# Optimization experiments

Measured on AMD Instinct MI355X. Metric: run time of the kernel, lower is better.

The kernel has to match this reference:

```python
import jax, jax.numpy as jnp
import numpy as np

N = 6144      # nodes
DIN = 65      # input_dim (1 time + 64 space coords)
DOUT = 65     # output_dim per head
H = 4         # nheads
EPS = 1e-7
MIN = 1e-15
# curvature c = 1 throughout (MultiHeadGraphAttentionLayer hardcodes curvature=1)

def arcosh(z):
    return jnp.log(z + jnp.sqrt(jnp.maximum(z * z - 1.0, 0.0)))

def hyp_proj(u):
    # project onto hyperboloid: recompute time coord
    y = u[..., 1:]
    t = jnp.sqrt(1.0 + jnp.sum(y * y, -1, keepdims=True))
    return jnp.concatenate([t, y], -1)

def expmap0(u):
    v = u[..., 1:]
    n = jnp.maximum(jnp.linalg.norm(v, axis=-1, keepdims=True), MIN)
    return jnp.concatenate([jnp.cosh(n), jnp.sinh(n) * v / n], -1)

def logmap0(x):
    y = x[..., 1:]
    n = jnp.maximum(jnp.linalg.norm(y, axis=-1, keepdims=True), MIN)
    t = jnp.maximum(x[..., :1], 1.0 + EPS)
    return jnp.concatenate([jnp.zeros_like(t), arcosh(t) * y / n], -1)

def hyp_linear(x, W):
    # HypLinear (use_bias=False, eval mode): mobius_matvec = exp0(log0(x) @ W^T), then proj
    return hyp_proj(expmap0(logmap0(x) @ W.T))

def to_poincare(x):
    return x[..., 1:] / (x[..., :1] + 1.0)

def to_hyperboloid(p):
    s = jnp.sum(p * p, -1, keepdims=True)
    return jnp.concatenate([1.0 + s, 2.0 * p], -1) / jnp.maximum(1.0 - s, MIN)

def mobius_half(v):
    # 0.5 (x) v  (mobius scalar multiplication, c=1)
    n = jnp.maximum(jnp.linalg.norm(v, axis=-1, keepdims=True), MIN)
    return jnp.tanh(0.5 * jnp.arctanh(jnp.minimum(n, 1.0 - EPS))) * v / n

def head(x, adj_t, Wa, Wd, Wo):
    att = hyp_linear(x, Wa)   # [N, DOUT]
    red = hyp_linear(x, Wd)   # [N, DOUT]
    # pairwise hyperboloid sqdist via Minkowski inner product (negate time coord)
    am = att.at[:, 0].multiply(-1.0)
    theta = jnp.maximum(-(am @ att.T), 1.0 + EPS)          # [N, N]
    S = jnp.minimum(arcosh(theta) ** 2, 50.0)
    # coef[i, j] = -adj[j, i] * sqdist for incoming edges (mask = adj^T)
    coef = jnp.where(adj_t > 0.01, -adj_t * S, 0.0)
    # F.normalize along incoming-edge axis (zeros don't change the L2 norm)
    a = coef / jnp.maximum(jnp.linalg.norm(coef, axis=-1, keepdims=True), 1e-12)
    pv = to_poincare(red)                                   # [N, DOUT-1]
    lam = 2.0 / jnp.maximum(1.0 - jnp.sum(pv * pv, -1), MIN)  # conformal factors [N]
    num = (a * lam[None, :]) @ pv                           # [N, DOUT-1]
    den = jnp.sum(jnp.abs(a) * (lam - 1.0)[None, :], -1, keepdims=True)
    m = mobius_half(num / jnp.maximum(den, MIN))            # mobius midpoint
    return hyp_linear(to_hyperboloid(m), Wo)                # [N, DOUT]

def reference(x, adj, W_att, W_data, W_out, W_lin):
    adj_t = adj.T
    hs = jnp.stack([head(x, adj_t, W_att[h], W_data[h], W_out[h]) for h in range(H)], axis=1)  # [N, H, DOUT]
    p = to_poincare(hs).reshape(x.shape[0], -1)             # PoincareBall.concat -> [N, H*(DOUT-1)]
    return hyp_linear(to_hyperboloid(p), W_lin)             # [N, H*DOUT]

def setup_inputs():
    key = jax.random.key(0)
    ks = jax.random.split(key, 8)
    sp = 0.1 * jax.random.normal(ks[0], (N, DIN - 1), jnp.float32)
    x = jnp.concatenate([jnp.sqrt(1.0 + jnp.sum(sp * sp, -1, keepdims=True)), sp], -1)
    adj = (jax.random.uniform(ks[1], (N, N)) < 32.0 / N).astype(jnp.float32)
    adj = jnp.maximum(adj, jnp.eye(N, dtype=jnp.float32))  # every node >=1 incoming edge
    def xavier(k, shape):
        b = (6.0 / (shape[0] + shape[1])) ** 0.5
        return jax.random.uniform(k, shape, jnp.float32, -b, b)
    W_att = jnp.stack([xavier(jax.random.fold_in(ks[2], h), (DOUT, DIN)) for h in range(H)])
    W_data = jnp.stack([xavier(jax.random.fold_in(ks[3], h), (DOUT, DIN)) for h in range(H)])
    W_out = jnp.stack([xavier(jax.random.fold_in(ks[4], h), (DOUT, DOUT)) for h in range(H)])
    W_lin = xavier(ks[5], (H * DOUT, H * (DOUT - 1) + 1))
    return {"x": x, "adj": adj, "W_att": W_att, "W_data": W_data, "W_out": W_out, "W_lin": W_lin}
```

## Files before the change

kernel.cpp:

```cpp
#include <hip/hip_runtime.h>
#include <math.h>

#define N 6144
#define H 4
#define CAP 128
#define MINF 1e-15f
#define ONE_EPS  1.0000001192092896f
#define ONE_MEPS 0.9999998807907104f

__device__ __forceinline__ float wave_reduce_sum(float v) {
    v += __shfl_xor(v, 32, 64);
    v += __shfl_xor(v, 16, 64);
    v += __shfl_xor(v, 8, 64);
    v += __shfl_xor(v, 4, 64);
    v += __shfl_xor(v, 2, 64);
    v += __shfl_xor(v, 1, 64);
    return v;
}

__device__ __forceinline__ float arcosh_f(float z) {
    return logf(z + sqrtf(fmaxf(z * z - 1.0f, 0.0f)));
}

__global__ void k_prep(const float* __restrict__ x, float* __restrict__ lmv,
                       const float* __restrict__ W_att, const float* __restrict__ W_data,
                       const float* __restrict__ W_out, const float* __restrict__ Wl,
                       float* __restrict__ Bp, float* __restrict__ Bo,
                       float* __restrict__ WlT, int* __restrict__ cnt) {
    int b = blockIdx.x;
    if (b < 1536) {
        int i = b * 4 + (threadIdx.x >> 6);
        int lane = threadIdx.x & 63;
        float y = x[i * 65 + 1 + lane];
        float ss = wave_reduce_sum(y * y);
        float n = fmaxf(sqrtf(ss), MINF);
        float t = fmaxf(x[i * 65], ONE_EPS);
        lmv[i * 64 + lane] = arcosh_f(t) * y / n;
    } else if (b < 1728) {
        int tid = (b - 1536) * 256 + threadIdx.x;
        int m = tid >> 12;
        int r = tid & 4095;
        int k = r >> 6, o = r & 63;
        const float* src;
        if (m < 4) src = W_att + m * 65 * 65;
        else if (m < 8) src = W_data + (m - 4) * 65 * 65;
        else src = W_out + (m - 8) * 65 * 65;
        float val = src[(1 + o) * 65 + (1 + k)];
        if (m < 8) Bp[m * 4096 + k * 64 + o] = val;
        else Bo[(m - 8) * 4096 + k * 64 + o] = val;
    } else if (b < 1808) {
        int L = ((b - 1728) * 256 + threadIdx.x) * 4;
        int k = L / 320, o0 = L % 320;
        float v[4];
        #pragma unroll
        for (int q = 0; q < 4; q++) {
            int o = o0 + q;
            v[q] = (o < 259) ? Wl[(size_t)(1 + o) * 257 + 1 + k] : 0.f;
        }
        *(float4*)(WlT + L) = make_float4(v[0], v[1], v[2], v[3]);
    } else {
        cnt[(b - 1808) * 256 + threadIdx.x] = 0;
    }
}

__global__ void __launch_bounds__(256) k_csr_gemm(
        const float* __restrict__ adj, int* __restrict__ cnt, int* __restrict__ idx,
        const float* __restrict__ lmv, const float* __restrict__ Bp,
        float* __restrict__ attv, float2* __restrict__ a0l, float* __restrict__ pv) {
    __shared__ float smem[64 * 65];
    if (blockIdx.x < 768) {
        float (*As)[64] = (float(*)[64])smem;
        float (*Bs)[64] = (float(*)[64])(smem + 1024);
        float (*Cs)[65] = (float(*)[65])smem;
        int my = blockIdx.x / 96;
        int ix = blockIdx.x % 96;
        const float* Bb = Bp + (size_t)my * 4096;
        int i0 = ix * 64;
        int tid = threadIdx.x;
        int tx = tid & 15, ty = tid >> 4;
        float acc[4][4] = {};
        for (int k0 = 0; k0 < 64; k0 += 16) {
            {
                int mm = tid >> 2, kq = tid & 3;
                float4 v = *(const float4*)(lmv + (size_t)(i0 + mm) * 64 + k0 + kq * 4);
                As[kq * 4 + 0][mm] = v.x;
                As[kq * 4 + 1][mm] = v.y;
                As[kq * 4 + 2][mm] = v.z;
                As[kq * 4 + 3][mm] = v.w;
            }
            {
                int kk = tid >> 4, o4 = tid & 15;
                float4 bvv = *(const float4*)(Bb + (k0 + kk) * 64 + o4 * 4);
                *(float4*)&Bs[kk][o4 * 4] = bvv;
            }
            __syncthreads();
            #pragma unroll
            for (int kk = 0; kk < 16; kk++) {
                float4 av = *(const float4*)&As[kk][ty * 4];
                float4 bv = *(const float4*)&Bs[kk][tx * 4];
                float a[4] = {av.x, av.y, av.z, av.w};
                float b[4] = {bv.x, bv.y, bv.z, bv.w};
                #pragma unroll
                for (int r = 0; r < 4; r++)
                    #pragma unroll
                    for (int c = 0; c < 4; c++) acc[r][c] += a[r] * b[c];
            }
            __syncthreads();
        }
        #pragma unroll
        for (int r = 0; r < 4; r++)
            #pragma unroll
            for (int c = 0; c < 4; c++)
                Cs[ty * 4 + r][tx * 4 + c] = acc[r][c];
        __syncthreads();
        int w = tid >> 6, lane = tid & 63;
        bool isAtt = my < 4;
        int h = my & 3;
        #pragma unroll 1
        for (int r = 0; r < 16; r++) {
            int row = w * 16 + r;
            int i = i0 + row;
            float u = Cs[row][lane];
            float nn = fmaxf(sqrtf(wave_reduce_sum(u * u)), MINF);
            if (isAtt) {
                float sha = sinhf(nn);
                attv[((size_t)h * N + i) * 64 + lane] = sha * u / nn;
                if (lane == 0) a0l[h * N + i].x = coshf(nn);
            } else {
                float shd = sinhf(nn), chd = coshf(nn);
                float pvd = (shd * u / nn) / (chd + 1.0f);
                pv[((size_t)h * N + i) * 64 + lane] = pvd;
                float sp = wave_reduce_sum(pvd * pvd);
                if (lane == 0) a0l[h * N + i].y = 2.0f / fmaxf(1.0f - sp, MINF);
            }
        }
    } else {
        const float4* a4 = (const float4*)adj;
        const unsigned STRIDE = 1048576u;
        unsigned e0 = (blockIdx.x - 768) * 256 + threadIdx.x;
        float4 v0 = a4[e0];
        float4 v1 = a4[e0 + STRIDE];
        #pragma unroll 1
        for (int it = 0; it < 9; it++) {
            float4 vn;
            if (it < 7) vn = a4[e0 + (unsigned)(it + 2) * STRIDE];
            unsigned base = (e0 + (unsigned)it * STRIDE) * 4u;
            float vals[4] = {v0.x, v0.y, v0.z, v0.w};
            #pragma unroll
            for (int q = 0; q < 4; q++) {
                if (vals[q] > 0.01f) {
                    unsigned t = base + q;
                    int j = t / N;
                    int i = t % N;
                    int pos = atomicAdd(&cnt[i], 1);
                    if (pos < CAP) idx[i * CAP + pos] = j;
                }
            }
            v0 = v1;
            v1 = vn;
        }
    }
}

__global__ void __launch_bounds__(256) k_attn(
        const int* __restrict__ cnt, const int* __restrict__ idx,
        const float* __restrict__ attv, const float2* __restrict__ a0l,
        const float* __restrict__ pv, float* __restrict__ lm2) {
    __shared__ float wls[4][CAP];
    __shared__ int jls[4][CAP];
    int w = threadIdx.x >> 6, lane = threadIdx.x & 63;
    int i = blockIdx.x * 4 + w;
    int h = blockIdx.y;
    const float* attvh = attv + (size_t)h * N * 64;
    const float* pvh = pv + (size_t)h * N * 64;
    const float2* a0lh = a0l + (size_t)h * N;

    int c = lane & 3;
    float4 aireg[4];
    #pragma unroll
    for (int q = 0; q < 4; q++)
        aireg[q] = *(const float4*)(attvh + (size_t)i * 64 + q * 16 + c * 4);
    float ai0 = a0lh[i].x;
    int nn = min(cnt[i], CAP);

    float accd = 0.f, accss = 0.f;
    for (int base = 0; base < nn; base += 16) {
        int t = base + (lane >> 2);
        bool act = t < nn;
        int j = act ? idx[i * CAP + t] : i;
        float2 al = a0lh[j];
        float d = 0.f;
        #pragma unroll
        for (int q = 0; q < 4; q++) {
            float4 b = *(const float4*)(attvh + (size_t)j * 64 + q * 16 + c * 4);
            float4 a = aireg[q];
            d += a.x * b.x + a.y * b.y + a.z * b.z + a.w * b.w;
        }
        d += __shfl_xor(d, 1, 64);
        d += __shfl_xor(d, 2, 64);
        float theta = fmaxf(ai0 * al.x - d, ONE_EPS);
        float ar = arcosh_f(theta);
        float S = fminf(ar * ar, 50.0f);
        if (!act) S = 0.f;
        if (c == 0) {
            accd += S * (al.y - 1.0f);
            accss += S * S;
            wls[w][t] = S * al.y;
            jls[w][t] = j;
        }
    }
    accd = wave_reduce_sum(accd);
    accss = wave_reduce_sum(accss);
    float nrm = fmaxf(sqrtf(accss), 1e-12f);
    float den = fmaxf(accd / nrm, MINF);
    float scl = 1.0f / (nrm * den);

    float accn = 0.f;
    #pragma unroll 4
    for (int t = 0; t < nn; t++) {
        int j = jls[w][t];
        float wq = wls[w][t];
        accn = fmaf(wq, pvh[(size_t)j * 64 + lane], accn);
    }
    float v = -scl * accn;
    float nv = fmaxf(sqrtf(wave_reduce_sum(v * v)), MINF);
    float nc = fminf(nv, ONE_MEPS);
    float mh = tanhf(0.5f * atanhf(nc));
    float md = mh * v / nv;
    float s = wave_reduce_sum(md * md);
    float Dh = fmaxf(1.0f - s, MINF);
    float hb0 = (1.0f + s) / Dh;
    float hbv = 2.0f * md / Dh;
    float nh = fmaxf(2.0f * sqrtf(s) / Dh, MINF);
    float t2 = fmaxf(hb0, ONE_EPS);
    lm2[((size_t)h * N + i) * 64 + lane] = arcosh_f(t2) * hbv / nh;
}

#define PS 272
#define BS5 336
__global__ void __launch_bounds__(256) k_tail(
        const float* __restrict__ lm2, const float* __restrict__ Bo,
        const float* __restrict__ WlT, float* __restrict__ out) {
    __shared__ float smem[5376 + 16 * PS];
    float* As1 = smem;
    float* Bs1 = smem + 1088;
    float* Bs5 = smem;
    float* P   = smem + 5376;

    int i0 = blockIdx.x * 16;
    int tid = threadIdx.x;
    int ty = tid >> 4;
    int tx = tid & 15;

    for (int h = 0; h < H; h++) {
        {
            float4 v = *(const float4*)(lm2 + ((size_t)h * N + i0 + ty) * 64 + tx * 4);
            *(float4*)(As1 + ty * 68 + tx * 4) = v;
        }
        float acc[4] = {0.f, 0.f, 0.f, 0.f};
        for (int k0 = 0; k0 < 64; k0 += 16) {
            {
                *(float4*)(Bs1 + ty * 64 + tx * 4) =
                    *(const float4*)(Bo + (size_t)h * 4096 + (k0 + ty) * 64 + tx * 4);
            }
            __syncthreads();
            #pragma unroll
            for (int kk = 0; kk < 16; kk++) {
                float a = As1[ty * 68 + k0 + kk];
                float4 bv = *(const float4*)(Bs1 + kk * 64 + tx * 4);
                acc[0] += a * bv.x;
                acc[1] += a * bv.y;
                acc[2] += a * bv.z;
                acc[3] += a * bv.w;
            }
            __syncthreads();
        }
        float ss = acc[0] * acc[0] + acc[1] * acc[1] + acc[2] * acc[2] + acc[3] * acc[3];
        ss += __shfl_xor(ss, 1, 64);
        ss += __shfl_xor(ss, 2, 64);
        ss += __shfl_xor(ss, 4, 64);
        ss += __shfl_xor(ss, 8, 64);
        float nn = fmaxf(sqrtf(ss), MINF);
        float sh = sinhf(nn), ch = coshf(nn);
        float* Pr = P + ty * PS + h * 64 + tx * 4;
        Pr[0] = (sh * acc[0] / nn) / (ch + 1.0f);
        Pr[1] = (sh * acc[1] / nn) / (ch + 1.0f);
        Pr[2] = (sh * acc[2] / nn) / (ch + 1.0f);
        Pr[3] = (sh * acc[3] / nn) / (ch + 1.0f);
    }
    __syncthreads();

    {
        float sp = 0.f;
        float4 pl[4];
        #pragma unroll
        for (int q = 0; q < 4; q++) {
            pl[q] = *(const float4*)(P + ty * PS + q * 64 + tx * 4);
            sp += pl[q].x * pl[q].x + pl[q].y * pl[q].y
                + pl[q].z * pl[q].z + pl[q].w * pl[q].w;
        }
        sp += __shfl_xor(sp, 1, 64);
        sp += __shfl_xor(sp, 2, 64);
        sp += __shfl_xor(sp, 4, 64);
        sp += __shfl_xor(sp, 8, 64);
        float Dh = fmaxf(1.0f - sp, MINF);
        float t2 = fmaxf((1.0f + sp) / Dh, ONE_EPS);
        float nh = fmaxf(2.0f * sqrtf(sp) / Dh, MINF);
        float ar2 = arcosh_f(t2);
        #pragma unroll
        for (int q = 0; q < 4; q++) {
            float4 v = pl[q];
            v.x = ar2 * (2.0f * v.x / Dh) / nh;
            v.y = ar2 * (2.0f * v.y / Dh) / nh;
            v.z = ar2 * (2.0f * v.z / Dh) / nh;
            v.w = ar2 * (2.0f * v.w / Dh) / nh;
            *(float4*)(P + ty * PS + q * 64 + tx * 4) = v;
        }
    }
    __syncthreads();

    float acc2[5][4] = {};
    for (int k0 = 0; k0 < 256; k0 += 16) {
        {
            #pragma unroll
            for (int q = 0; q < 5; q++)
                *(float4*)(Bs5 + ty * BS5 + q * 64 + tx * 4) =
                    *(const float4*)(WlT + (size_t)(k0 + ty) * 320 + q * 64 + tx * 4);
        }
        __syncthreads();
        #pragma unroll
        for (int kq = 0; kq < 4; kq++) {
            float4 pv4 = *(const float4*)(P + ty * PS + k0 + kq * 4);
            float av[4] = {pv4.x, pv4.y, pv4.z, pv4.w};
            #pragma unroll
            for (int j = 0; j < 4; j++) {
                float a = av[j];
                int kk = kq * 4 + j;
                #pragma unroll
                for (int q = 0; q < 5; q++) {
                    float4 bv = *(const float4*)(Bs5 + kk * BS5 + q * 64 + tx * 4);
                    acc2[q][0] += a * bv.x;
                    acc2[q][1] += a * bv.y;
                    acc2[q][2] += a * bv.z;
                    acc2[q][3] += a * bv.w;
                }
            }
        }
        __syncthreads();
    }

    float ss2 = 0.f;
    #pragma unroll
    for (int q = 0; q < 5; q++)
        ss2 += acc2[q][0] * acc2[q][0] + acc2[q][1] * acc2[q][1]
             + acc2[q][2] * acc2[q][2] + acc2[q][3] * acc2[q][3];
    ss2 += __shfl_xor(ss2, 1, 64);
    ss2 += __shfl_xor(ss2, 2, 64);
    ss2 += __shfl_xor(ss2, 4, 64);
    ss2 += __shfl_xor(ss2, 8, 64);
    float nv = fmaxf(sqrtf(ss2), MINF);
    float sh2 = sinhf(nv);
    float scale = sh2 / nv;
    size_t ob = (size_t)(i0 + ty) * 260;
    #pragma unroll
    for (int q = 0; q < 4; q++) {
        int o = q * 64 + tx * 4;
        out[ob + 1 + o + 0] = scale * acc2[q][0];
        out[ob + 1 + o + 1] = scale * acc2[q][1];
        out[ob + 1 + o + 2] = scale * acc2[q][2];
        out[ob + 1 + o + 3] = scale * acc2[q][3];
    }
    if (tx == 0) {
        out[ob] = sqrtf(1.0f + sh2 * sh2);
        out[ob + 257] = scale * acc2[4][0];
        out[ob + 258] = scale * acc2[4][1];
        out[ob + 259] = scale * acc2[4][2];
    }
}

extern "C" void kernel_launch(void* const* d_in, const int* in_sizes, int n_in,
                              void* d_out, int out_size, void* d_ws, size_t ws_size,
                              hipStream_t stream) {
    const float* x = (const float*)d_in[0];
    const float* adj = (const float*)d_in[1];
    const float* W_att = (const float*)d_in[2];
    const float* W_data = (const float*)d_in[3];
    const float* W_out = (const float*)d_in[4];
    const float* W_lin = (const float*)d_in[5];
    float* out = (float*)d_out;

    char* ws = (char*)d_ws;
    size_t off = 0;
    auto alloc = [&](size_t bytes) {
        void* ptr = ws + off;
        off += (bytes + 255) & ~(size_t)255;
        return ptr;
    };
    int* cnt = (int*)alloc((size_t)N * 4);
    int* idx = (int*)alloc((size_t)N * CAP * 4);
    float* lmv = (float*)alloc((size_t)N * 64 * 4);
    float* attv = (float*)alloc((size_t)H * N * 64 * 4);
    float2* a0l = (float2*)alloc((size_t)H * N * 8);
    float* pvb = (float*)alloc((size_t)H * N * 64 * 4);
    float* lm2 = (float*)alloc((size_t)H * N * 64 * 4);
    float* Bp = (float*)alloc((size_t)8 * 4096 * 4);
    float* Bo = (float*)alloc((size_t)4 * 4096 * 4);
    float* WlT = (float*)alloc((size_t)256 * 320 * 4);

    k_prep<<<1832, 256, 0, stream>>>(x, lmv, W_att, W_data, W_out, W_lin,
                                     Bp, Bo, WlT, cnt);
    k_csr_gemm<<<4864, 256, 0, stream>>>(adj, cnt, idx, lmv, Bp, attv, a0l, pvb);
    k_attn<<<dim3(N / 4, H), 256, 0, stream>>>(cnt, idx, attv, a0l, pvb, lm2);
    k_tail<<<N / 16, 256, 0, stream>>>(lm2, Bo, WlT, out);
}
```

Measured before the change: 322.0 us.

## Fuse attention aggregation into one pass over fp16 interleaved key/value rows

Stores the attention vectors and Poincaré values as fp16 in one interleaved 128-half row per node, so each neighbour gather reads both in a single contiguous row. The separate second loop over neighbours, with its shared-memory weight lists, is replaced by per-lane 16-wide partial accumulators. These are combined with a butterfly transpose-reduce whose bit-reversed output order is undone by permuting the W_out rows in prep. Blocks are also remapped so adjacent blocks share a head, and self-edges get zero weight explicitly. The goal is to halve gather traffic and remove a dependent second pass, at the cost of fp16 rounding and more registers per thread.

```diff
diff --git a/kernel.cpp b/kernel.cpp
--- a/kernel.cpp
+++ b/kernel.cpp
@@ -1,4 +1,5 @@
 #include <hip/hip_runtime.h>
+#include <hip/hip_fp16.h>
 #include <math.h>
 
 #define N 6144
@@ -20,6 +21,20 @@
 
 __device__ __forceinline__ float arcosh_f(float z) {
     return logf(z + sqrtf(fmaxf(z * z - 1.0f, 0.0f)));
+}
+
+__device__ __forceinline__ void h8_to_f(float4 r, float* o) {
+    __half2* h = (__half2*)&r;
+    #pragma unroll
+    for (int q = 0; q < 4; q++) {
+        float2 f = __half22float2(h[q]);
+        o[2 * q + 0] = f.x;
+        o[2 * q + 1] = f.y;
+    }
+}
+
+__device__ __forceinline__ int bitrev4(int t) {
+    return ((t & 1) << 3) | ((t & 2) << 1) | ((t & 4) >> 1) | ((t & 8) >> 3);
 }
 
 __global__ void k_prep(const float* __restrict__ x, float* __restrict__ lmv,
@@ -45,9 +60,12 @@
         if (m < 4) src = W_att + m * 65 * 65;
         else if (m < 8) src = W_data + (m - 4) * 65 * 65;
         else src = W_out + (m - 8) * 65 * 65;
-        float val = src[(1 + o) * 65 + (1 + k)];
-        if (m < 8) Bp[m * 4096 + k * 64 + o] = val;
-        else Bo[(m - 8) * 4096 + k * 64 + o] = val;
+        if (m < 8) {
+            Bp[m * 4096 + k * 64 + o] = src[(1 + o) * 65 + (1 + k)];
+        } else {
+            int dk = (k & 3) * 16 + bitrev4(k >> 2);
+            Bo[(m - 8) * 4096 + k * 64 + o] = src[(1 + o) * 65 + (1 + dk)];
+        }
     } else if (b < 1808) {
         int L = ((b - 1728) * 256 + threadIdx.x) * 4;
         int k = L / 320, o0 = L % 320;
@@ -66,7 +84,7 @@
 __global__ void __launch_bounds__(256) k_csr_gemm(
         const float* __restrict__ adj, int* __restrict__ cnt, int* __restrict__ idx,
         const float* __restrict__ lmv, const float* __restrict__ Bp,
-        float* __restrict__ attv, float2* __restrict__ a0l, float* __restrict__ pv) {
+        __half* __restrict__ kv, float2* __restrict__ a0l) {
     __shared__ float smem[64 * 65];
     if (blockIdx.x < 768) {
         float (*As)[64] = (float(*)[64])smem;
@@ -124,12 +142,12 @@
             float nn = fmaxf(sqrtf(wave_reduce_sum(u * u)), MINF);
             if (isAtt) {
                 float sha = sinhf(nn);
-                attv[((size_t)h * N + i) * 64 + lane] = sha * u / nn;
+                kv[((size_t)h * N + i) * 128 + lane] = __float2half(sha * u / nn);
                 if (lane == 0) a0l[h * N + i].x = coshf(nn);
             } else {
                 float shd = sinhf(nn), chd = coshf(nn);
                 float pvd = (shd * u / nn) / (chd + 1.0f);
-                pv[((size_t)h * N + i) * 64 + lane] = pvd;
+                kv[((size_t)h * N + i) * 128 + 64 + lane] = __float2half(pvd);
                 float sp = wave_reduce_sum(pvd * pvd);
                 if (lane == 0) a0l[h * N + i].y = 2.0f / fmaxf(1.0f - sp, MINF);
             }
@@ -164,50 +182,62 @@
 
 __global__ void __launch_bounds__(256) k_attn(
         const int* __restrict__ cnt, const int* __restrict__ idx,
-        const float* __restrict__ attv, const float2* __restrict__ a0l,
-        const float* __restrict__ pv, float* __restrict__ lm2) {
-    __shared__ float wls[4][CAP];
-    __shared__ int jls[4][CAP];
+        const __half* __restrict__ kv, const float2* __restrict__ a0l,
+        float* __restrict__ lm2) {
     int w = threadIdx.x >> 6, lane = threadIdx.x & 63;
-    int i = blockIdx.x * 4 + w;
-    int h = blockIdx.y;
-    const float* attvh = attv + (size_t)h * N * 64;
-    const float* pvh = pv + (size_t)h * N * 64;
+    int gb = blockIdx.x;
+    int slot = gb & 7;
+    int h = slot >> 1;
+    int iblk = (gb >> 3) * 2 + (slot & 1);
+    int i = iblk * 4 + w;
+
+    const __half* kvh = kv + (size_t)h * N * 128;
     const float2* a0lh = a0l + (size_t)h * N;
-
-    int c = lane & 3;
-    float4 aireg[4];
-    #pragma unroll
-    for (int q = 0; q < 4; q++)
-        aireg[q] = *(const float4*)(attvh + (size_t)i * 64 + q * 16 + c * 4);
+    int c = lane & 3, t = lane >> 2;
+
+    float ai[16];
+    {
+        float4 r0 = *(const float4*)(kvh + (size_t)i * 128 + c * 16);
+        float4 r1 = *(const float4*)(kvh + (size_t)i * 128 + c * 16 + 8);
+        h8_to_f(r0, ai);
+        h8_to_f(r1, ai + 8);
+    }
     float ai0 = a0lh[i].x;
     int nn = min(cnt[i], CAP);
 
     float accd = 0.f, accss = 0.f;
+    float accn16[16] = {};
     for (int base = 0; base < nn; base += 16) {
-        int t = base + (lane >> 2);
-        bool act = t < nn;
-        int j = act ? idx[i * CAP + t] : i;
+        int tt = base + t;
+        bool act = tt < nn;
+        int j = act ? idx[i * CAP + tt] : i;
         float2 al = a0lh[j];
+        const __half* row = kvh + (size_t)j * 128;
+        float4 b0 = *(const float4*)(row + c * 16);
+        float4 b1 = *(const float4*)(row + c * 16 + 8);
+        float4 p0 = *(const float4*)(row + 64 + c * 16);
+        float4 p1 = *(const float4*)(row + 64 + c * 16 + 8);
+        float bv[16], pw[16];
+        h8_to_f(b0, bv);
+        h8_to_f(b1, bv + 8);
+        h8_to_f(p0, pw);
+        h8_to_f(p1, pw + 8);
         float d = 0.f;
         #pragma unroll
-        for (int q = 0; q < 4; q++) {
-            float4 b = *(const float4*)(attvh + (size_t)j * 64 + q * 16 + c * 4);
-            float4 a = aireg[q];
-            d += a.x * b.x + a.y * b.y + a.z * b.z + a.w * b.w;
-        }
+        for (int k = 0; k < 16; k++) d += ai[k] * bv[k];
         d += __shfl_xor(d, 1, 64);
         d += __shfl_xor(d, 2, 64);
         float theta = fmaxf(ai0 * al.x - d, ONE_EPS);
         float ar = arcosh_f(theta);
         float S = fminf(ar * ar, 50.0f);
-        if (!act) S = 0.f;
+        if (!act || j == i) S = 0.f;
+        float wq = S * al.y;
         if (c == 0) {
             accd += S * (al.y - 1.0f);
             accss += S * S;
-            wls[w][t] = S * al.y;
-            jls[w][t] = j;
-        }
+        }
+        #pragma unroll
+        for (int k = 0; k < 16; k++) accn16[k] = fmaf(wq, pw[k], accn16[k]);
     }
     accd = wave_reduce_sum(accd);
     accss = wave_reduce_sum(accss);
@@ -215,14 +245,45 @@
     float den = fmaxf(accd / nrm, MINF);
     float scl = 1.0f / (nrm * den);
 
-    float accn = 0.f;
-    #pragma unroll 4
-    for (int t = 0; t < nn; t++) {
-        int j = jls[w][t];
-        float wq = wls[w][t];
-        accn = fmaf(wq, pvh[(size_t)j * 64 + lane], accn);
-    }
-    float v = -scl * accn;
+    float r8[8];
+    {
+        bool b0 = t & 1;
+        #pragma unroll
+        for (int kk = 0; kk < 8; kk++) {
+            float mine = b0 ? accn16[kk + 8] : accn16[kk];
+            float send = b0 ? accn16[kk] : accn16[kk + 8];
+            r8[kk] = mine + __shfl_xor(send, 4, 64);
+        }
+    }
+    float r4[4];
+    {
+        bool b1 = t & 2;
+        #pragma unroll
+        for (int kk = 0; kk < 4; kk++) {
+            float mine = b1 ? r8[kk + 4] : r8[kk];
+            float send = b1 ? r8[kk] : r8[kk + 4];
+            r4[kk] = mine + __shfl_xor(send, 8, 64);
+        }
+    }
+    float r2[2];
+    {
+        bool b2 = t & 4;
+        #pragma unroll
+        for (int kk = 0; kk < 2; kk++) {
+            float mine = b2 ? r4[kk + 2] : r4[kk];
+            float send = b2 ? r4[kk] : r4[kk + 2];
+            r2[kk] = mine + __shfl_xor(send, 16, 64);
+        }
+    }
+    float r1;
+    {
+        bool b3 = t & 8;
+        float mine = b3 ? r2[1] : r2[0];
+        float send = b3 ? r2[0] : r2[1];
+        r1 = mine + __shfl_xor(send, 32, 64);
+    }
+
+    float v = -scl * r1;
     float nv = fmaxf(sqrtf(wave_reduce_sum(v * v)), MINF);
     float nc = fminf(nv, ONE_MEPS);
     float mh = tanhf(0.5f * atanhf(nc));
@@ -399,9 +460,8 @@
     int* cnt = (int*)alloc((size_t)N * 4);
     int* idx = (int*)alloc((size_t)N * CAP * 4);
     float* lmv = (float*)alloc((size_t)N * 64 * 4);
-    float* attv = (float*)alloc((size_t)H * N * 64 * 4);
+    __half* kv = (__half*)alloc((size_t)H * N * 128 * 2);
     float2* a0l = (float2*)alloc((size_t)H * N * 8);
-    float* pvb = (float*)alloc((size_t)H * N * 64 * 4);
     float* lm2 = (float*)alloc((size_t)H * N * 64 * 4);
     float* Bp = (float*)alloc((size_t)8 * 4096 * 4);
     float* Bo = (float*)alloc((size_t)4 * 4096 * 4);
@@ -409,7 +469,7 @@
 
     k_prep<<<1832, 256, 0, stream>>>(x, lmv, W_att, W_data, W_out, W_lin,
                                      Bp, Bo, WlT, cnt);
-    k_csr_gemm<<<4864, 256, 0, stream>>>(adj, cnt, idx, lmv, Bp, attv, a0l, pvb);
-    k_attn<<<dim3(N / 4, H), 256, 0, stream>>>(cnt, idx, attv, a0l, pvb, lm2);
+    k_csr_gemm<<<4864, 256, 0, stream>>>(adj, cnt, idx, lmv, Bp, kv, a0l);
+    k_attn<<<6144, 256, 0, stream>>>(cnt, idx, kv, a0l, lm2);
     k_tail<<<N / 16, 256, 0, stream>>>(lm2, Bo, WlT, out);
 }
```

Result: faster. 313.9 us (-2.5%).
